# Performance work log

Hardware: AMD Instinct MI355X
Metric: run time of the kernel (lower is better)

The kernel has to match this reference:

```python
import jax, jax.numpy as jnp
import numpy as np

N_TOKENS = 16384
IN_FEATURES = 1024
OUT_FEATURES = 1024
BH = 32  # block rows (out dim)
BW = 32  # block cols (in dim)
N_BLOCKS = 256  # density 0.25 * (1024*1024/(32*32))


def setup_inputs() -> dict:
    key = jax.random.key(0)
    k1, k2, k3, k4 = jax.random.split(key, 4)
    x = jax.random.normal(k1, (N_TOKENS, IN_FEATURES), dtype=jnp.float32)
    weight_data = jax.random.normal(k2, (N_BLOCKS, BH, BW), dtype=jnp.float32)
    bias = jnp.zeros((OUT_FEATURES,), dtype=jnp.float32)
    block_row = jax.random.randint(k3, (N_BLOCKS,), 0, OUT_FEATURES // BH, dtype=jnp.int32)
    block_col = jax.random.randint(k4, (N_BLOCKS,), 0, IN_FEATURES // BW, dtype=jnp.int32)
    return {"x": x, "weight_data": weight_data, "bias": bias,
            "block_row": block_row, "block_col": block_col}


def reference(x, weight_data, bias, block_row, block_col):
    # Block-sparse linear: y = x @ W^T + bias, with W[out, in] stored as
    # N_BLOCKS dense (BH, BW) blocks at (block_row, block_col) block coords.
    N = x.shape[0]
    B, bh, bw = weight_data.shape
    n_row_blocks = bias.shape[0] // bh
    x3 = x.reshape(N, -1, bw)           # [N, in/bw, bw]
    xb = x3[:, block_col, :]            # gather input block-columns: [N, B, bw]
    # per-block partial output rows: data[b] @ x_colblock -> [N, B, bh]
    partial = jnp.einsum('nbw,bow->nbo', xb, weight_data)
    y3 = jnp.zeros((N, n_row_blocks, bh), dtype=x.dtype).at[:, block_row, :].add(partial)
    return y3.reshape(N, -1) + bias
```

## Files before the change

kernel.cpp:

```cpp
#include <hip/hip_runtime.h>

#define N_TOKENS 16384
#define IN_F 1024
#define OUT_F 1024
#define NB 256
#define BH 32
#define BW 32
#define NRB 32
#define T_TILE 16
#define XS_STRIDE 1032
#define MAX_SCHED (NB + NRB)
#define WF_SLOT_SHORTS 1024

#define WS_WF_BYTES   (MAX_SCHED * WF_SLOT_SHORTS * 2)
#define WS_SCHED_OFF  WS_WF_BYTES
#define WS_POS_OFF    (WS_SCHED_OFF + MAX_SCHED * 4)
#define WS_WSTART_OFF (WS_POS_OFF + NB * 4)

typedef short short8 __attribute__((ext_vector_type(8)));
typedef float float4v __attribute__((ext_vector_type(4)));

__device__ __forceinline__ short f2bf(float f) {
    unsigned u = __builtin_bit_cast(unsigned, f);
    u += 0x7fffu + ((u >> 16) & 1u);
    return (short)(u >> 16);
}

__global__ void prep_sched_kernel(const int* __restrict__ brow, const int* __restrict__ bcol,
                                  int* __restrict__ sched, int* __restrict__ pos_of,
                                  int* __restrict__ wstart, short* __restrict__ wf)
{
    __shared__ int sr[NB], sc[NB], scnt[NRB];
    const int tid = threadIdx.x;
    for (int i = tid; i < NB; i += 64) { sr[i] = brow[i]; sc[i] = bcol[i]; }
    __syncthreads();
    if (tid < NRB) {
        int c = 0;
        for (int b = 0; b < NB; ++b) c += (sr[b] == tid);
        scnt[tid] = c;
    }
    __syncthreads();
    if (tid < NRB) {
        const int r = tid, w = r & 3, i = r >> 2;
        int start = 0;
        for (int rr = 0; rr < NRB; ++rr) {
            const int ww = rr & 3, ii = rr >> 2;
            const int adj = scnt[rr] > 0 ? scnt[rr] : 1;
            if (ww < w || (ww == w && ii < i)) start += adj;
        }
        int pos = start;
        const int cnt = scnt[r];
        if (cnt == 0) {
            sched[pos] = (r << 5) | (1 << 10);
            int4 z = {0, 0, 0, 0};
            int4* dst = (int4*)(wf + (size_t)pos * WF_SLOT_SHORTS);
            for (int q = 0; q < WF_SLOT_SHORTS / 8; ++q) dst[q] = z;
        } else {
            int emitted = 0;
            for (int b = 0; b < NB; ++b) {
                if (sr[b] == r) {
                    ++emitted;
                    const int fl = (emitted == cnt) ? (1 << 10) : 0;
                    sched[pos] = sc[b] | (r << 5) | fl;
                    pos_of[b] = pos;
                    ++pos;
                }
            }
        }
    }
    if (tid < 5) {
        int acc = 0;
        for (int rr = 0; rr < NRB; ++rr) {
            const int adj = scnt[rr] > 0 ? scnt[rr] : 1;
            if ((rr & 3) < tid) acc += adj;
        }
        wstart[tid] = acc;
    }
}

__global__ void prep_w_kernel(const float* __restrict__ wd, const int* __restrict__ pos_of,
                              short* __restrict__ wf)
{
    const int g = blockIdx.x * blockDim.x + threadIdx.x;
    const int lane = g & 63;
    const int oh = (g >> 6) & 1;
    const int b = g >> 7;
    const int l16 = lane & 15, quad = lane >> 4;
    const int pos = pos_of[b];
    const float* src = wd + (size_t)b * (BH * BW) + (oh * 16 + l16) * BW + quad * 8;
    const float4 w0 = *(const float4*)src;
    const float4 w1 = *(const float4*)(src + 4);
    short8 o;
    o[0] = f2bf(w0.x); o[1] = f2bf(w0.y); o[2] = f2bf(w0.z); o[3] = f2bf(w0.w);
    o[4] = f2bf(w1.x); o[5] = f2bf(w1.y); o[6] = f2bf(w1.z); o[7] = f2bf(w1.w);
    *(short8*)(wf + (((size_t)pos * 2 + oh) * 64 + lane) * 8) = o;
}

__global__ __launch_bounds__(256, 4) void spmm_main_kernel(
    const float* __restrict__ x, const float* __restrict__ bias,
    const short* __restrict__ wf, const int* __restrict__ sched_g,
    const int* __restrict__ wstart_g, float* __restrict__ out)
{
    __shared__ short xs[T_TILE * XS_STRIDE];
    __shared__ int ssched[MAX_SCHED];
    __shared__ int swstart[5];

    const int tid = threadIdx.x;
    const int n0 = blockIdx.x * T_TILE;

    {
        const int tr = tid >> 7;
        const int tc = tid & 127;
        const float* xp = x + (size_t)(n0 + tr) * IN_F + tc * 8;
        short* sp = xs + tr * XS_STRIDE + tc * 8;
#pragma unroll
        for (int it = 0; it < T_TILE / 2; ++it) {
            const float4 a = *(const float4*)xp;
            const float4 b = *(const float4*)(xp + 4);
            short8 s;
            s[0] = f2bf(a.x); s[1] = f2bf(a.y); s[2] = f2bf(a.z); s[3] = f2bf(a.w);
            s[4] = f2bf(b.x); s[5] = f2bf(b.y); s[6] = f2bf(b.z); s[7] = f2bf(b.w);
            *(short8*)sp = s;
            xp += 2 * IN_F;
            sp += 2 * XS_STRIDE;
        }
    }
    ssched[tid] = sched_g[tid];
    if (tid < MAX_SCHED - 256) ssched[256 + tid] = sched_g[256 + tid];
    if (tid < 5) swstart[tid] = wstart_g[tid];
    __syncthreads();

    const int lane = tid & 63;
    const int wave = tid >> 6;
    const int l16 = lane & 15, quad = lane >> 4;

    const int s = swstart[wave];
    const int e = swstart[wave + 1];

    const short* xrow = xs + l16 * XS_STRIDE + quad * 8;
    const short* wfl = wf + lane * 8;

    int e0 = ssched[s];
    int e1 = ssched[(s + 1 < MAX_SCHED) ? s + 1 : MAX_SCHED - 1];
    short8 a0 = *(const short8*)(xrow + (e0 & 31) * BW);
    short8 wA0 = *(const short8*)(wfl + (size_t)(s * 2 + 0) * 512);
    short8 wB0 = *(const short8*)(wfl + (size_t)(s * 2 + 1) * 512);
    const int p1 = (s + 1 < e) ? s + 1 : e - 1;
    short8 wA1 = *(const short8*)(wfl + (size_t)(p1 * 2 + 0) * 512);
    short8 wB1 = *(const short8*)(wfl + (size_t)(p1 * 2 + 1) * 512);

    float4v acc0 = {0.f, 0.f, 0.f, 0.f};
    float4v acc1 = {0.f, 0.f, 0.f, 0.f};

    for (int k = s; k < e; ++k) {
        const int kp = (k + 2 < e) ? k + 2 : e - 1;
        const int ei = (k + 2 < MAX_SCHED) ? k + 2 : MAX_SCHED - 1;
        const int ep = ssched[ei];
        short8 wA2 = *(const short8*)(wfl + (size_t)(kp * 2 + 0) * 512);
        short8 wB2 = *(const short8*)(wfl + (size_t)(kp * 2 + 1) * 512);
        short8 a1 = *(const short8*)(xrow + (e1 & 31) * BW);

        acc0 = __builtin_amdgcn_mfma_f32_16x16x32_bf16(a0, wA0, acc0, 0, 0, 0);
        acc1 = __builtin_amdgcn_mfma_f32_16x16x32_bf16(a0, wB0, acc1, 0, 0, 0);

        if (e0 & (1 << 10)) {
            const int r = (e0 >> 5) & 31;
            const int ob = r * BH + l16;
            const float bv0 = bias[ob];
            const float bv1 = bias[ob + 16];
            float* op = out + (size_t)(n0 + quad * 4) * OUT_F + ob;
#pragma unroll
            for (int g = 0; g < 4; ++g) {
                op[g * OUT_F] = acc0[g] + bv0;
                op[g * OUT_F + 16] = acc1[g] + bv1;
            }
            acc0 = (float4v){0.f, 0.f, 0.f, 0.f};
            acc1 = (float4v){0.f, 0.f, 0.f, 0.f};
        }
        e0 = e1; e1 = ep;
        a0 = a1;
        wA0 = wA1; wB0 = wB1;
        wA1 = wA2; wB1 = wB2;
    }
}

extern "C" void kernel_launch(void* const* d_in, const int* in_sizes, int n_in,
                              void* d_out, int out_size, void* d_ws, size_t ws_size,
                              hipStream_t stream) {
    const float* x    = (const float*)d_in[0];
    const float* wd   = (const float*)d_in[1];
    const float* bias = (const float*)d_in[2];
    const int* brow   = (const int*)d_in[3];
    const int* bcol   = (const int*)d_in[4];
    float* out = (float*)d_out;

    char* ws = (char*)d_ws;
    short* wf     = (short*)ws;
    int* sched    = (int*)(ws + WS_SCHED_OFF);
    int* pos_of   = (int*)(ws + WS_POS_OFF);
    int* wstart   = (int*)(ws + WS_WSTART_OFF);

    prep_sched_kernel<<<1, 64, 0, stream>>>(brow, bcol, sched, pos_of, wstart, wf);
    prep_w_kernel<<<NB * 128 / 256, 256, 0, stream>>>(wd, pos_of, wf);
    spmm_main_kernel<<<N_TOKENS / T_TILE, 256, 0, stream>>>(x, bias, wf, sched, wstart, out);
}
```

Before: 164.3 us.

## Double token tile to reuse weight fragments across two MFMA rows; parallelize schedule prep

The main kernel now processes 32 tokens per block instead of 16. Each wave issues four MFMAs per schedule step, so every loaded weight fragment feeds two token halves, halving global weight traffic per token and the number of blocks. The schedule prep kernel now uses 256 threads with shared-memory atomics instead of serial loops. Bias is preloaded per output row, and the schedule is padded to remove bounds clamps. The trade-off is higher LDS and register use per block, with the launch bound reduced to 2 blocks per CU, which lowers occupancy.

```diff
diff --git a/kernel.cpp b/kernel.cpp
--- a/kernel.cpp
+++ b/kernel.cpp
@@ -7,14 +7,15 @@
 #define BH 32
 #define BW 32
 #define NRB 32
-#define T_TILE 16
-#define XS_STRIDE 1032
+#define T_TILE 32
+#define XS_STRIDE 1040
 #define MAX_SCHED (NB + NRB)
+#define SCHED_PAD (MAX_SCHED + 2)
 #define WF_SLOT_SHORTS 1024
 
-#define WS_WF_BYTES   (MAX_SCHED * WF_SLOT_SHORTS * 2)
+#define WS_WF_BYTES   (SCHED_PAD * WF_SLOT_SHORTS * 2)
 #define WS_SCHED_OFF  WS_WF_BYTES
-#define WS_POS_OFF    (WS_SCHED_OFF + MAX_SCHED * 4)
+#define WS_POS_OFF    (WS_SCHED_OFF + SCHED_PAD * 4)
 #define WS_WSTART_OFF (WS_POS_OFF + NB * 4)
 
 typedef short short8 __attribute__((ext_vector_type(8)));
@@ -30,51 +31,43 @@
                                   int* __restrict__ sched, int* __restrict__ pos_of,
                                   int* __restrict__ wstart, short* __restrict__ wf)
 {
-    __shared__ int sr[NB], sc[NB], scnt[NRB];
+    __shared__ int cnt[NRB], start[NRB], cur[NRB];
     const int tid = threadIdx.x;
-    for (int i = tid; i < NB; i += 64) { sr[i] = brow[i]; sc[i] = bcol[i]; }
+    if (tid < NRB) { cnt[tid] = 0; cur[tid] = 0; }
+    __syncthreads();
+    const int r = brow[tid];
+    const int c = bcol[tid];
+    atomicAdd(&cnt[r], 1);
     __syncthreads();
     if (tid < NRB) {
-        int c = 0;
-        for (int b = 0; b < NB; ++b) c += (sr[b] == tid);
-        scnt[tid] = c;
-    }
-    __syncthreads();
-    if (tid < NRB) {
-        const int r = tid, w = r & 3, i = r >> 2;
-        int start = 0;
+        const int w = tid & 3, i = tid >> 2;
+        int s = 0;
         for (int rr = 0; rr < NRB; ++rr) {
+            const int adj = cnt[rr] > 0 ? cnt[rr] : 1;
             const int ww = rr & 3, ii = rr >> 2;
-            const int adj = scnt[rr] > 0 ? scnt[rr] : 1;
-            if (ww < w || (ww == w && ii < i)) start += adj;
-        }
-        int pos = start;
-        const int cnt = scnt[r];
-        if (cnt == 0) {
-            sched[pos] = (r << 5) | (1 << 10);
-            int4 z = {0, 0, 0, 0};
-            int4* dst = (int4*)(wf + (size_t)pos * WF_SLOT_SHORTS);
-            for (int q = 0; q < WF_SLOT_SHORTS / 8; ++q) dst[q] = z;
-        } else {
-            int emitted = 0;
-            for (int b = 0; b < NB; ++b) {
-                if (sr[b] == r) {
-                    ++emitted;
-                    const int fl = (emitted == cnt) ? (1 << 10) : 0;
-                    sched[pos] = sc[b] | (r << 5) | fl;
-                    pos_of[b] = pos;
-                    ++pos;
-                }
-            }
-        }
-    }
-    if (tid < 5) {
-        int acc = 0;
+            if (ww < w || (ww == w && ii < i)) s += adj;
+        }
+        start[tid] = s;
+    }
+    if (tid >= 64 && tid < 69) {
+        const int w = tid - 64;
+        int s = 0;
         for (int rr = 0; rr < NRB; ++rr) {
-            const int adj = scnt[rr] > 0 ? scnt[rr] : 1;
-            if ((rr & 3) < tid) acc += adj;
-        }
-        wstart[tid] = acc;
+            const int adj = cnt[rr] > 0 ? cnt[rr] : 1;
+            if ((rr & 3) < w) s += adj;
+        }
+        wstart[w] = s;
+    }
+    __syncthreads();
+    const int slot = atomicAdd(&cur[r], 1);
+    const int pos = start[r] + slot;
+    sched[pos] = c | (r << 5) | ((slot == cnt[r] - 1) ? (1 << 10) : 0);
+    pos_of[tid] = pos;
+    if (tid < NRB && cnt[tid] == 0) {
+        sched[start[tid]] = (tid << 5) | (1 << 10);
+        int4 z = {0, 0, 0, 0};
+        int4* dst = (int4*)(wf + (size_t)start[tid] * WF_SLOT_SHORTS);
+        for (int q = 0; q < WF_SLOT_SHORTS / 8; ++q) dst[q] = z;
     }
 }
 
@@ -93,16 +86,16 @@
     short8 o;
     o[0] = f2bf(w0.x); o[1] = f2bf(w0.y); o[2] = f2bf(w0.z); o[3] = f2bf(w0.w);
     o[4] = f2bf(w1.x); o[5] = f2bf(w1.y); o[6] = f2bf(w1.z); o[7] = f2bf(w1.w);
-    *(short8*)(wf + (((size_t)pos * 2 + oh) * 64 + lane) * 8) = o;
-}
-
-__global__ __launch_bounds__(256, 4) void spmm_main_kernel(
+    *(short8*)(wf + (size_t)pos * WF_SLOT_SHORTS + oh * 512 + lane * 8) = o;
+}
+
+__global__ __launch_bounds__(256, 2) void spmm_main_kernel(
     const float* __restrict__ x, const float* __restrict__ bias,
     const short* __restrict__ wf, const int* __restrict__ sched_g,
     const int* __restrict__ wstart_g, float* __restrict__ out)
 {
     __shared__ short xs[T_TILE * XS_STRIDE];
-    __shared__ int ssched[MAX_SCHED];
+    __shared__ int ssched[SCHED_PAD];
     __shared__ int swstart[5];
 
     const int tid = threadIdx.x;
@@ -126,7 +119,7 @@
         }
     }
     ssched[tid] = sched_g[tid];
-    if (tid < MAX_SCHED - 256) ssched[256 + tid] = sched_g[256 + tid];
+    if (tid < SCHED_PAD - 256) ssched[256 + tid] = sched_g[256 + tid];
     if (tid < 5) swstart[tid] = wstart_g[tid];
     __syncthreads();
 
@@ -137,48 +130,62 @@
     const int s = swstart[wave];
     const int e = swstart[wave + 1];
 
-    const short* xrow = xs + l16 * XS_STRIDE + quad * 8;
+    const short* x0 = xs + l16 * XS_STRIDE + quad * 8;
+    const short* x1 = xs + (16 + l16) * XS_STRIDE + quad * 8;
     const short* wfl = wf + lane * 8;
 
     int e0 = ssched[s];
-    int e1 = ssched[(s + 1 < MAX_SCHED) ? s + 1 : MAX_SCHED - 1];
-    short8 a0 = *(const short8*)(xrow + (e0 & 31) * BW);
-    short8 wA0 = *(const short8*)(wfl + (size_t)(s * 2 + 0) * 512);
-    short8 wB0 = *(const short8*)(wfl + (size_t)(s * 2 + 1) * 512);
-    const int p1 = (s + 1 < e) ? s + 1 : e - 1;
-    short8 wA1 = *(const short8*)(wfl + (size_t)(p1 * 2 + 0) * 512);
-    short8 wB1 = *(const short8*)(wfl + (size_t)(p1 * 2 + 1) * 512);
-
-    float4v acc0 = {0.f, 0.f, 0.f, 0.f};
-    float4v acc1 = {0.f, 0.f, 0.f, 0.f};
+    int e1 = ssched[s + 1];
+    short8 a0_0 = *(const short8*)(x0 + (e0 & 31) * BW);
+    short8 a0_1 = *(const short8*)(x1 + (e0 & 31) * BW);
+    short8 wA0 = *(const short8*)(wfl + (size_t)s * WF_SLOT_SHORTS);
+    short8 wB0 = *(const short8*)(wfl + (size_t)s * WF_SLOT_SHORTS + 512);
+    short8 wA1 = *(const short8*)(wfl + (size_t)(s + 1) * WF_SLOT_SHORTS);
+    short8 wB1 = *(const short8*)(wfl + (size_t)(s + 1) * WF_SLOT_SHORTS + 512);
+
+    int rn = wave;
+    float bv0 = bias[rn * BH + l16];
+    float bv1 = bias[rn * BH + 16 + l16];
+
+    float4v acc00 = {0.f, 0.f, 0.f, 0.f};
+    float4v acc01 = {0.f, 0.f, 0.f, 0.f};
+    float4v acc10 = {0.f, 0.f, 0.f, 0.f};
+    float4v acc11 = {0.f, 0.f, 0.f, 0.f};
 
     for (int k = s; k < e; ++k) {
-        const int kp = (k + 2 < e) ? k + 2 : e - 1;
-        const int ei = (k + 2 < MAX_SCHED) ? k + 2 : MAX_SCHED - 1;
-        const int ep = ssched[ei];
-        short8 wA2 = *(const short8*)(wfl + (size_t)(kp * 2 + 0) * 512);
-        short8 wB2 = *(const short8*)(wfl + (size_t)(kp * 2 + 1) * 512);
-        short8 a1 = *(const short8*)(xrow + (e1 & 31) * BW);
-
-        acc0 = __builtin_amdgcn_mfma_f32_16x16x32_bf16(a0, wA0, acc0, 0, 0, 0);
-        acc1 = __builtin_amdgcn_mfma_f32_16x16x32_bf16(a0, wB0, acc1, 0, 0, 0);
+        const int ep = ssched[k + 2];
+        const short8 wA2 = *(const short8*)(wfl + (size_t)(k + 2) * WF_SLOT_SHORTS);
+        const short8 wB2 = *(const short8*)(wfl + (size_t)(k + 2) * WF_SLOT_SHORTS + 512);
+        const short8 a1_0 = *(const short8*)(x0 + (e1 & 31) * BW);
+        const short8 a1_1 = *(const short8*)(x1 + (e1 & 31) * BW);
+
+        acc00 = __builtin_amdgcn_mfma_f32_16x16x32_bf16(a0_0, wA0, acc00, 0, 0, 0);
+        acc01 = __builtin_amdgcn_mfma_f32_16x16x32_bf16(a0_0, wB0, acc01, 0, 0, 0);
+        acc10 = __builtin_amdgcn_mfma_f32_16x16x32_bf16(a0_1, wA0, acc10, 0, 0, 0);
+        acc11 = __builtin_amdgcn_mfma_f32_16x16x32_bf16(a0_1, wB0, acc11, 0, 0, 0);
 
         if (e0 & (1 << 10)) {
             const int r = (e0 >> 5) & 31;
             const int ob = r * BH + l16;
-            const float bv0 = bias[ob];
-            const float bv1 = bias[ob + 16];
-            float* op = out + (size_t)(n0 + quad * 4) * OUT_F + ob;
+            float* op0 = out + (size_t)(n0 + quad * 4) * OUT_F + ob;
+            float* op1 = out + (size_t)(n0 + 16 + quad * 4) * OUT_F + ob;
 #pragma unroll
             for (int g = 0; g < 4; ++g) {
-                op[g * OUT_F] = acc0[g] + bv0;
-                op[g * OUT_F + 16] = acc1[g] + bv1;
+                op0[g * OUT_F]      = acc00[g] + bv0;
+                op0[g * OUT_F + 16] = acc01[g] + bv1;
+                op1[g * OUT_F]      = acc10[g] + bv0;
+                op1[g * OUT_F + 16] = acc11[g] + bv1;
             }
-            acc0 = (float4v){0.f, 0.f, 0.f, 0.f};
-            acc1 = (float4v){0.f, 0.f, 0.f, 0.f};
+            acc00 = (float4v){0.f, 0.f, 0.f, 0.f};
+            acc01 = (float4v){0.f, 0.f, 0.f, 0.f};
+            acc10 = (float4v){0.f, 0.f, 0.f, 0.f};
+            acc11 = (float4v){0.f, 0.f, 0.f, 0.f};
+            rn = (rn + 4) & 31;
+            bv0 = bias[rn * BH + l16];
+            bv1 = bias[rn * BH + 16 + l16];
         }
         e0 = e1; e1 = ep;
-        a0 = a1;
+        a0_0 = a1_0; a0_1 = a1_1;
         wA0 = wA1; wB0 = wB1;
         wA1 = wA2; wB1 = wB2;
     }
@@ -195,12 +202,12 @@
     float* out = (float*)d_out;
 
     char* ws = (char*)d_ws;
-    short* wf     = (short*)ws;
-    int* sched    = (int*)(ws + WS_SCHED_OFF);
-    int* pos_of   = (int*)(ws + WS_POS_OFF);
-    int* wstart   = (int*)(ws + WS_WSTART_OFF);
-
-    prep_sched_kernel<<<1, 64, 0, stream>>>(brow, bcol, sched, pos_of, wstart, wf);
+    short* wf   = (short*)ws;
+    int* sched  = (int*)(ws + WS_SCHED_OFF);
+    int* pos_of = (int*)(ws + WS_POS_OFF);
+    int* wstart = (int*)(ws + WS_WSTART_OFF);
+
+    prep_sched_kernel<<<1, 256, 0, stream>>>(brow, bcol, sched, pos_of, wstart, wf);
     prep_w_kernel<<<NB * 128 / 256, 256, 0, stream>>>(wd, pos_of, wf);
     spmm_main_kernel<<<N_TOKENS / T_TILE, 256, 0, stream>>>(x, bias, wf, sched, wstart, out);
 }
```

After: 137.4 us. -16.4%, faster.
